# Kernel tuning notes

Hardware: AMD Instinct MI355X
Metric: run time of the kernel (lower is better)

## Reference

```python
import jax, jax.numpy as jnp
import numpy as np

HADAMARD_DIM = 4096  # power of 2


def _sylvester_hadamard(n: int) -> np.ndarray:
    # Matches the torch recursion: H_n = [[H, H], [H, -H]] (Sylvester ordering).
    H = np.ones((1, 1), dtype=np.float32)
    while H.shape[0] < n:
        H = np.block([[H, H], [H, -H]])
    return H


def setup_inputs() -> dict:
    key = jax.random.key(0)
    x = jax.random.normal(key, (8192, HADAMARD_DIM), dtype=jnp.float32)
    return {"x": x}


def reference(x) -> jnp.ndarray:
    # Faithful to forward: x @ hadamard_matrix (group_size=-1, force_fp32=False).
    # The dense matmul is the math being computed; a kernel may replace it with
    # an O(n log n) fast Walsh-Hadamard transform (Sylvester ordering).
    H = jnp.asarray(_sylvester_hadamard(HADAMARD_DIM))  # [D, D]
    return x @ H  # [N, D]
```

## Files before the change

### kernel.cpp

```cpp
#include <hip/hip_runtime.h>

#define HAD_D 4096
#define PER_THREAD 64
#define NVEC 16

typedef float floatx4 __attribute__((ext_vector_type(4)));

__global__ __launch_bounds__(256) void fwht4096_kernel(const float* __restrict__ x,
                                                       float* __restrict__ out,
                                                       int nrows) {
    const int wave = threadIdx.x >> 6;
    const int lane = threadIdx.x & 63;
    const int row  = blockIdx.x * 4 + wave;
    if (row >= nrows) return;

    const floatx4* __restrict__ x4 = (const floatx4*)(x + (size_t)row * HAD_D);
    floatx4* __restrict__ y4       = (floatx4*)(out + (size_t)row * HAD_D);

    float v[PER_THREAD];

    #pragma unroll
    for (int k = 0; k < NVEC; ++k) {
        floatx4 t = x4[k * 64 + lane];
        v[4*k+0] = t.x; v[4*k+1] = t.y; v[4*k+2] = t.z; v[4*k+3] = t.w;
    }

    #pragma unroll
    for (int k = 0; k < NVEC; ++k) {
        float a = v[4*k+0], b = v[4*k+1], c = v[4*k+2], d = v[4*k+3];
        float a1 = a + b, b1 = a - b, c1 = c + d, d1 = c - d;
        v[4*k+0] = a1 + c1;
        v[4*k+1] = b1 + d1;
        v[4*k+2] = a1 - c1;
        v[4*k+3] = b1 - d1;
    }

    #pragma unroll
    for (int s = 1; s <= 32; s <<= 1) {
        const bool upper = (lane & s) != 0;
        #pragma unroll
        for (int j = 0; j < PER_THREAD; ++j) {
            float partner = __shfl_xor(v[j], s, 64);
            v[j] = upper ? (partner - v[j]) : (v[j] + partner);
        }
    }

    #pragma unroll
    for (int s = 1; s <= 8; s <<= 1) {
        #pragma unroll
        for (int k = 0; k < NVEC; ++k) {
            if ((k & s) == 0) {
                #pragma unroll
                for (int m = 0; m < 4; ++m) {
                    float a = v[4*k+m], b = v[4*(k+s)+m];
                    v[4*k+m]     = a + b;
                    v[4*(k+s)+m] = a - b;
                }
            }
        }
    }

    #pragma unroll
    for (int k = 0; k < NVEC; ++k) {
        floatx4 t;
        t.x = v[4*k+0]; t.y = v[4*k+1]; t.z = v[4*k+2]; t.w = v[4*k+3];
        __builtin_nontemporal_store(t, y4 + k * 64 + lane);
    }
}

extern "C" void kernel_launch(void* const* d_in, const int* in_sizes, int n_in,
                              void* d_out, int out_size, void* d_ws, size_t ws_size,
                              hipStream_t stream) {
    const float* x = (const float*)d_in[0];
    float* out     = (float*)d_out;
    const int nrows = in_sizes[0] / HAD_D;
    const int blocks = (nrows + 3) / 4;
    hipLaunchKernelGGL(fwht4096_kernel, dim3(blocks), dim3(256), 0, stream,
                       x, out, nrows);
}
```

Measured before the change: 47.58 us.

## Replace cross-lane shuffles with swizzled LDS transpose and DPP butterflies

Replaces the six rounds of 64 shuffle-xor butterflies with a swizzled LDS transpose: in-register stages run first, data is redistributed through shared memory so most remaining stages are also in-register, and the last two stages use DPP quad permutes. Work per block drops to two rows with 128 threads and 32KB of LDS. The aim is to remove the heavy ds_bpermute/shuffle instruction cost. In exchange it adds LDS traffic, block syncs and lower occupancy from the LDS use, and it drops the row bounds check, assuming an even row count.

```diff
diff --git a/kernel.cpp b/kernel.cpp
--- a/kernel.cpp
+++ b/kernel.cpp
@@ -1,70 +1,116 @@
 #include <hip/hip_runtime.h>
 
 #define HAD_D 4096
-#define PER_THREAD 64
-#define NVEC 16
 
 typedef float floatx4 __attribute__((ext_vector_type(4)));
 
-__global__ __launch_bounds__(256) void fwht4096_kernel(const float* __restrict__ x,
+__device__ __forceinline__ float dpp_xor1(float x) {
+    return __builtin_bit_cast(float,
+        __builtin_amdgcn_mov_dpp(__builtin_bit_cast(int, x), 0xB1, 0xF, 0xF, true));
+}
+__device__ __forceinline__ float dpp_xor2(float x) {
+    return __builtin_bit_cast(float,
+        __builtin_amdgcn_mov_dpp(__builtin_bit_cast(int, x), 0x4E, 0xF, 0xF, true));
+}
+
+__global__ __launch_bounds__(128) void fwht4096_kernel(const float* __restrict__ x,
                                                        float* __restrict__ out,
                                                        int nrows) {
+    __shared__ __align__(16) float lds[2 * HAD_D];
     const int wave = threadIdx.x >> 6;
     const int lane = threadIdx.x & 63;
-    const int row  = blockIdx.x * 4 + wave;
-    if (row >= nrows) return;
+    const int row  = blockIdx.x * 2 + wave;
+    float* wlds = lds + wave * HAD_D;
 
     const floatx4* __restrict__ x4 = (const floatx4*)(x + (size_t)row * HAD_D);
     floatx4* __restrict__ y4       = (floatx4*)(out + (size_t)row * HAD_D);
 
-    float v[PER_THREAD];
+    floatx4 v[16];
+    #pragma unroll
+    for (int k = 0; k < 16; ++k) v[k] = x4[k * 64 + lane];
 
     #pragma unroll
-    for (int k = 0; k < NVEC; ++k) {
-        floatx4 t = x4[k * 64 + lane];
-        v[4*k+0] = t.x; v[4*k+1] = t.y; v[4*k+2] = t.z; v[4*k+3] = t.w;
+    for (int k = 0; k < 16; ++k) {
+        float a = v[k].x, b = v[k].y, c = v[k].z, d = v[k].w;
+        float a1 = a + b, b1 = a - b, c1 = c + d, d1 = c - d;
+        v[k].x = a1 + c1; v[k].y = b1 + d1; v[k].z = a1 - c1; v[k].w = b1 - d1;
+    }
+    #pragma unroll
+    for (int s = 1; s <= 8; s <<= 1) {
+        #pragma unroll
+        for (int k = 0; k < 16; ++k) {
+            if ((k & s) == 0) {
+                floatx4 a = v[k], b = v[k ^ s];
+                v[k] = a + b; v[k ^ s] = a - b;
+            }
+        }
     }
 
+    const int t2     = lane >> 4;
+    const int pibase = (t2 << 4) | (lane & 8);
+    const int xl     = (lane & 7) ^ (t2 << 1);
     #pragma unroll
-    for (int k = 0; k < NVEC; ++k) {
-        float a = v[4*k+0], b = v[4*k+1], c = v[4*k+2], d = v[4*k+3];
-        float a1 = a + b, b1 = a - b, c1 = c + d, d1 = c - d;
-        v[4*k+0] = a1 + c1;
-        v[4*k+1] = b1 + d1;
-        v[4*k+2] = a1 - c1;
-        v[4*k+3] = b1 - d1;
+    for (int k = 0; k < 16; ++k) {
+        int pi = pibase | (xl ^ (k & 1));
+        *(floatx4*)(wlds + k * 256 + pi * 4) = v[k];
     }
+    __syncthreads();
 
+    const int K      = lane >> 2;
+    const int t      = lane & 3;
+    const int rebase = K * 256;
+    const int rxor   = (t << 1) | (K & 1);
+    floatx4 w[16];
     #pragma unroll
-    for (int s = 1; s <= 32; s <<= 1) {
-        const bool upper = (lane & s) != 0;
-        #pragma unroll
-        for (int j = 0; j < PER_THREAD; ++j) {
-            float partner = __shfl_xor(v[j], s, 64);
-            v[j] = upper ? (partner - v[j]) : (v[j] + partner);
-        }
+    for (int u = 0; u < 16; ++u) {
+        int pi = (t << 4) | (u & 8) | ((u & 7) ^ rxor);
+        w[u] = *(const floatx4*)(wlds + rebase + pi * 4);
     }
 
     #pragma unroll
     for (int s = 1; s <= 8; s <<= 1) {
         #pragma unroll
-        for (int k = 0; k < NVEC; ++k) {
-            if ((k & s) == 0) {
-                #pragma unroll
-                for (int m = 0; m < 4; ++m) {
-                    float a = v[4*k+m], b = v[4*(k+s)+m];
-                    v[4*k+m]     = a + b;
-                    v[4*(k+s)+m] = a - b;
-                }
+        for (int u = 0; u < 16; ++u) {
+            if ((u & s) == 0) {
+                floatx4 a = w[u], b = w[u ^ s];
+                w[u] = a + b; w[u ^ s] = a - b;
             }
         }
     }
 
+    {
+        const float s1 = (lane & 1) ? -1.f : 1.f;
+        #pragma unroll
+        for (int u = 0; u < 16; ++u) {
+            w[u].x = fmaf(s1, w[u].x, dpp_xor1(w[u].x));
+            w[u].y = fmaf(s1, w[u].y, dpp_xor1(w[u].y));
+            w[u].z = fmaf(s1, w[u].z, dpp_xor1(w[u].z));
+            w[u].w = fmaf(s1, w[u].w, dpp_xor1(w[u].w));
+        }
+    }
+    {
+        const float s2 = (lane & 2) ? -1.f : 1.f;
+        #pragma unroll
+        for (int u = 0; u < 16; ++u) {
+            w[u].x = fmaf(s2, w[u].x, dpp_xor2(w[u].x));
+            w[u].y = fmaf(s2, w[u].y, dpp_xor2(w[u].y));
+            w[u].z = fmaf(s2, w[u].z, dpp_xor2(w[u].z));
+            w[u].w = fmaf(s2, w[u].w, dpp_xor2(w[u].w));
+        }
+    }
+
     #pragma unroll
-    for (int k = 0; k < NVEC; ++k) {
-        floatx4 t;
-        t.x = v[4*k+0]; t.y = v[4*k+1]; t.z = v[4*k+2]; t.w = v[4*k+3];
-        __builtin_nontemporal_store(t, y4 + k * 64 + lane);
+    for (int u = 0; u < 16; ++u) {
+        int pi = (t << 4) | (u & 8) | ((u & 7) ^ rxor);
+        *(floatx4*)(wlds + rebase + pi * 4) = w[u];
+    }
+    __syncthreads();
+
+    #pragma unroll
+    for (int k = 0; k < 16; ++k) {
+        int pi = pibase | (xl ^ (k & 1));
+        floatx4 o = *(const floatx4*)(wlds + k * 256 + pi * 4);
+        __builtin_nontemporal_store(o, y4 + k * 64 + lane);
     }
 }
 
@@ -74,7 +120,7 @@
     const float* x = (const float*)d_in[0];
     float* out     = (float*)d_out;
     const int nrows = in_sizes[0] / HAD_D;
-    const int blocks = (nrows + 3) / 4;
-    hipLaunchKernelGGL(fwht4096_kernel, dim3(blocks), dim3(256), 0, stream,
+    const int blocks = nrows / 2;
+    hipLaunchKernelGGL(fwht4096_kernel, dim3(blocks), dim3(128), 0, stream,
                        x, out, nrows);
 }
```

New measurement: 47.73 us. No clear change (+0.3%).
